# Kernel tuning notes

Hardware: AMD Instinct MI355X
Metric: run time of the kernel (lower is better)

## Reference

```python
import jax, jax.numpy as jnp
import numpy as np

N = 16384
D_IN = 128
D_OUT = 128
BETA = 1.0


def setup_inputs() -> dict:
    key = jax.random.key(0)
    k1, k2, k3 = jax.random.split(key, 3)
    x = jax.random.normal(k1, (N, D_IN), dtype=jnp.float32)
    adj = jax.random.uniform(k2, (N, N), dtype=jnp.float32)
    # single-layer MLP (mlp_layers=1 -> channels=[in_dim, out_dim] -> one Linear)
    W_mlp = jax.random.normal(k3, (D_IN, D_OUT), dtype=jnp.float32) * (1.0 / np.sqrt(D_IN))
    b_mlp = jnp.zeros((D_OUT,), dtype=jnp.float32)
    return {"x": x, "adj": adj, "W_mlp": W_mlp, "b_mlp": b_mlp}


def reference(x, adj, W_mlp, b_mlp):
    # softmax aggregator: attention = softmax(adj * beta, axis=-1); x = attention @ x
    attention = jax.nn.softmax(adj * BETA, axis=-1)  # [N, N]
    h = jnp.matmul(attention, x)                      # [N, D_IN]
    # MLP with a single linear layer
    out = jnp.matmul(h, W_mlp) + b_mlp                # [N, D_OUT]
    return out
```

## Files before the change

kernel.cpp:

```cpp
#include <hip/hip_runtime.h>
#include <hip/hip_bf16.h>


typedef short  short8  __attribute__((ext_vector_type(8)));
typedef float  floatx4 __attribute__((ext_vector_type(4)));

#define NN 16384
#define DD 128

__device__ __forceinline__ short f2bf(float f) {
    unsigned u = __float_as_uint(f);
    u += 0x7fff + ((u >> 16) & 1);
    return (short)(u >> 16);
}

__global__ __launch_bounds__(256, 2) void xw_kernel(
    const float* __restrict__ x, const float* __restrict__ W, short* __restrict__ yT)
{
    __shared__ short WT[128 * 136];
    const int t  = threadIdx.x;
    const int j0 = blockIdx.x * 64;

    #pragma unroll
    for (int i = 0; i < 16; ++i) {
        int f4 = t + 256 * i;
        int d = f4 >> 5, c4 = f4 & 31;
        float4 v = ((const float4*)W)[f4];
        WT[(4*c4 + 0) * 136 + d] = f2bf(v.x);
        WT[(4*c4 + 1) * 136 + d] = f2bf(v.y);
        WT[(4*c4 + 2) * 136 + d] = f2bf(v.z);
        WT[(4*c4 + 3) * 136 + d] = f2bf(v.w);
    }
    __syncthreads();

    const int lane = t & 63, w = t >> 6;
    const int nl = lane & 15, q = lane >> 4;
    const int j = j0 + 16 * w + nl;
    const float* xrow = x + (size_t)j * DD + 8 * q;

    floatx4 acc[8];
    #pragma unroll
    for (int kt = 0; kt < 8; ++kt) acc[kt] = (floatx4){0.f, 0.f, 0.f, 0.f};

    #pragma unroll
    for (int dstep = 0; dstep < 4; ++dstep) {
        float4 v0 = *(const float4*)(xrow + 32 * dstep);
        float4 v1 = *(const float4*)(xrow + 32 * dstep + 4);
        short8 bf;
        bf[0] = f2bf(v0.x); bf[1] = f2bf(v0.y); bf[2] = f2bf(v0.z); bf[3] = f2bf(v0.w);
        bf[4] = f2bf(v1.x); bf[5] = f2bf(v1.y); bf[6] = f2bf(v1.z); bf[7] = f2bf(v1.w);
        #pragma unroll
        for (int kt = 0; kt < 8; ++kt) {
            short8 af = *(const short8*)(&WT[(16*kt + nl) * 136 + 32*dstep + 8*q]);
            acc[kt] = __builtin_amdgcn_mfma_f32_16x16x32_bf16(af, bf, acc[kt], 0, 0, 0);
        }
    }
    #pragma unroll
    for (int kt = 0; kt < 8; ++kt) {
        #pragma unroll
        for (int r = 0; r < 4; ++r)
            yT[(size_t)(16*kt + 4*q + r) * NN + j] = f2bf(acc[kt][r]);
    }
}

__global__ __launch_bounds__(256, 1) void attn_kernel(
    const float* __restrict__ adj, const short* __restrict__ yT,
    const float* __restrict__ bias, float* __restrict__ out)
{
    const int t  = threadIdx.x;
    const int la = t & 63, w = t >> 6;
    const int m = la & 15, q = la >> 4;
    const int i0 = blockIdx.x * 64 + 16 * w;

    const float* aptr = adj + (size_t)(i0 + m) * NN + 8 * q;
    const short* bptr = yT + (size_t)m * NN + 8 * q;

    floatx4 acc[8];
    #pragma unroll
    for (int nt = 0; nt < 8; ++nt) acc[nt] = (floatx4){0.f, 0.f, 0.f, 0.f};
    float psumA = 0.f, psumB = 0.f;

    float4 A00, A01, A10, A11;
    uint4  B0[8], B1[8];

    auto load_slot = [&](int s, float4& Aa, float4& Ab, uint4* B) {
        const float* ap = aptr + (size_t)s * 32;
        Aa = *(const float4*)ap;
        Ab = *(const float4*)(ap + 4);
        const short* bp = bptr + (size_t)s * 32;
        #pragma unroll
        for (int nt = 0; nt < 8; ++nt)
            B[nt] = *(const uint4*)(bp + (size_t)nt * (16 * NN));
    };
    auto step = [&](const float4& Aa, const float4& Ab, const uint4* B, float& psum) {
        float e0 = __expf(Aa.x), e1 = __expf(Aa.y), e2 = __expf(Aa.z), e3 = __expf(Aa.w);
        float e4 = __expf(Ab.x), e5 = __expf(Ab.y), e6 = __expf(Ab.z), e7 = __expf(Ab.w);
        psum += ((e0 + e1) + (e2 + e3)) + ((e4 + e5) + (e6 + e7));
        short8 af;
        af[0] = f2bf(e0); af[1] = f2bf(e1); af[2] = f2bf(e2); af[3] = f2bf(e3);
        af[4] = f2bf(e4); af[5] = f2bf(e5); af[6] = f2bf(e6); af[7] = f2bf(e7);
        #pragma unroll
        for (int nt = 0; nt < 8; ++nt) {
            short8 bf = *(const short8*)&B[nt];
            acc[nt] = __builtin_amdgcn_mfma_f32_16x16x32_bf16(af, bf, acc[nt], 0, 0, 0);
        }
    };

    load_slot(0, A00, A01, B0);
    load_slot(1, A10, A11, B1);
    #pragma unroll 1
    for (int s = 0; s < NN / 32; s += 2) {
        step(A00, A01, B0, psumA);
        if (s + 2 < NN / 32) load_slot(s + 2, A00, A01, B0);
        step(A10, A11, B1, psumB);
        if (s + 3 < NN / 32) load_slot(s + 3, A10, A11, B1);
    }

    float sum = psumA + psumB;
    sum += __shfl_xor(sum, 16);
    sum += __shfl_xor(sum, 32);
    float inv = 1.0f / sum;
    float invr[4];
    #pragma unroll
    for (int r = 0; r < 4; ++r) invr[r] = __shfl(inv, 4 * q + r);

    #pragma unroll
    for (int nt = 0; nt < 8; ++nt) {
        float bv = bias[16 * nt + m];
        #pragma unroll
        for (int r = 0; r < 4; ++r)
            out[(size_t)(i0 + 4 * q + r) * DD + 16 * nt + m] = acc[nt][r] * invr[r] + bv;
    }
}

extern "C" void kernel_launch(void* const* d_in, const int* in_sizes, int n_in,
                              void* d_out, int out_size, void* d_ws, size_t ws_size,
                              hipStream_t stream)
{
    const float* x    = (const float*)d_in[0];
    const float* adj  = (const float*)d_in[1];
    const float* W    = (const float*)d_in[2];
    const float* bias = (const float*)d_in[3];
    float* out = (float*)d_out;
    short* yT  = (short*)d_ws;

    hipLaunchKernelGGL(xw_kernel,   dim3(256), dim3(256), 0, stream, x, W, yT);
    hipLaunchKernelGGL(attn_kernel, dim3(256), dim3(256), 0, stream, adj, yT, bias, out);
}
```

Measured before the change: 1.759 ms.

## Split attention K dimension across warps with shared-memory reduction for more blocks

```diff
diff --git a/kernel.cpp b/kernel.cpp
--- a/kernel.cpp
+++ b/kernel.cpp
@@ -7,6 +7,8 @@
 
 #define NN 16384
 #define DD 128
+#define KCH (NN / 4)
+#define KST (KCH / 32)
 
 __device__ __forceinline__ short f2bf(float f) {
     unsigned u = __float_as_uint(f);
@@ -63,17 +65,21 @@
     }
 }
 
-__global__ __launch_bounds__(256, 1) void attn_kernel(
+__global__ __launch_bounds__(256, 4) void attn_kernel(
     const float* __restrict__ adj, const short* __restrict__ yT,
     const float* __restrict__ bias, float* __restrict__ out)
 {
+    __shared__ float redA[32 * 64];
+    __shared__ float redB[32 * 64];
+    __shared__ float rsum[4][16];
+
     const int t  = threadIdx.x;
     const int la = t & 63, w = t >> 6;
     const int m = la & 15, q = la >> 4;
-    const int i0 = blockIdx.x * 64 + 16 * w;
+    const int i0 = blockIdx.x * 16;
 
-    const float* aptr = adj + (size_t)(i0 + m) * NN + 8 * q;
-    const short* bptr = yT + (size_t)m * NN + 8 * q;
+    const float* aptr = adj + (size_t)(i0 + m) * NN + w * KCH + 8 * q;
+    const short* bptr = yT + (size_t)m * NN + w * KCH + 8 * q;
 
     floatx4 acc[8];
     #pragma unroll
@@ -109,27 +115,71 @@
     load_slot(0, A00, A01, B0);
     load_slot(1, A10, A11, B1);
     #pragma unroll 1
-    for (int s = 0; s < NN / 32; s += 2) {
+    for (int s = 0; s < KST; s += 2) {
         step(A00, A01, B0, psumA);
-        if (s + 2 < NN / 32) load_slot(s + 2, A00, A01, B0);
+        if (s + 2 < KST) load_slot(s + 2, A00, A01, B0);
         step(A10, A11, B1, psumB);
-        if (s + 3 < NN / 32) load_slot(s + 3, A10, A11, B1);
+        if (s + 3 < KST) load_slot(s + 3, A10, A11, B1);
     }
 
     float sum = psumA + psumB;
     sum += __shfl_xor(sum, 16);
     sum += __shfl_xor(sum, 32);
-    float inv = 1.0f / sum;
-    float invr[4];
-    #pragma unroll
-    for (int r = 0; r < 4; ++r) invr[r] = __shfl(inv, 4 * q + r);
+    if (la < 16) rsum[w][la] = sum;
 
-    #pragma unroll
-    for (int nt = 0; nt < 8; ++nt) {
-        float bv = bias[16 * nt + m];
+    if (w == 2) {
         #pragma unroll
-        for (int r = 0; r < 4; ++r)
-            out[(size_t)(i0 + 4 * q + r) * DD + 16 * nt + m] = acc[nt][r] * invr[r] + bv;
+        for (int nt = 0; nt < 8; ++nt)
+            #pragma unroll
+            for (int r = 0; r < 4; ++r) redA[(nt * 4 + r) * 64 + la] = acc[nt][r];
+    }
+    if (w == 3) {
+        #pragma unroll
+        for (int nt = 0; nt < 8; ++nt)
+            #pragma unroll
+            for (int r = 0; r < 4; ++r) redB[(nt * 4 + r) * 64 + la] = acc[nt][r];
+    }
+    __syncthreads();
+    if (w == 0) {
+        #pragma unroll
+        for (int nt = 0; nt < 8; ++nt)
+            #pragma unroll
+            for (int r = 0; r < 4; ++r) acc[nt][r] += redA[(nt * 4 + r) * 64 + la];
+    }
+    if (w == 1) {
+        #pragma unroll
+        for (int nt = 0; nt < 8; ++nt)
+            #pragma unroll
+            for (int r = 0; r < 4; ++r) acc[nt][r] += redB[(nt * 4 + r) * 64 + la];
+    }
+    __syncthreads();
+    if (w == 1) {
+        #pragma unroll
+        for (int nt = 0; nt < 8; ++nt)
+            #pragma unroll
+            for (int r = 0; r < 4; ++r) redA[(nt * 4 + r) * 64 + la] = acc[nt][r];
+    }
+    __syncthreads();
+    if (w == 0) {
+        #pragma unroll
+        for (int nt = 0; nt < 8; ++nt)
+            #pragma unroll
+            for (int r = 0; r < 4; ++r) acc[nt][r] += redA[(nt * 4 + r) * 64 + la];
+
+        float invr[4];
+        #pragma unroll
+        for (int r = 0; r < 4; ++r) {
+            int row = 4 * q + r;
+            invr[r] = 1.0f / (rsum[0][row] + rsum[1][row] + rsum[2][row] + rsum[3][row]);
+        }
+
+        #pragma unroll
+        for (int nt = 0; nt < 8; ++nt) {
+            float bv = bias[16 * nt + m];
+            #pragma unroll
+            for (int r = 0; r < 4; ++r)
+                out[(size_t)(i0 + 4 * q + r) * DD + 16 * nt + m] = acc[nt][r] * invr[r] + bv;
+        }
     }
 }
 
@@ -144,6 +194,6 @@
     float* out = (float*)d_out;
     short* yT  = (short*)d_ws;
 
-    hipLaunchKernelGGL(xw_kernel,   dim3(256), dim3(256), 0, stream, x, W, yT);
-    hipLaunchKernelGGL(attn_kernel, dim3(256), dim3(256), 0, stream, adj, yT, bias, out);
+    hipLaunchKernelGGL(xw_kernel,   dim3(256),  dim3(256), 0, stream, x, W, yT);
+    hipLaunchKernelGGL(attn_kernel, dim3(1024), dim3(256), 0, stream, adj, yT, bias, out);
 }
```

Result: slower. 2.051 ms (+16.5%).
